# Kernel optimization log

Hardware: AMD Instinct MI355X
Metric: run time of the kernel (lower is better)

## Reference

```python
import jax, jax.numpy as jnp
import numpy as np

H = 100
EPS = 1e-5


def _ln(x, g, b):
    m = jnp.mean(x, axis=-1, keepdims=True)
    v = jnp.mean((x - m) ** 2, axis=-1, keepdims=True)
    return (x - m) / jnp.sqrt(v + EPS) * g + b


def _enc(x, W, b, g, be):
    # Linear -> Tanh -> LayerNorm
    return _ln(jnp.tanh(x @ W + b), g, be)


def setup_inputs() -> dict:
    key = jax.random.key(0)
    ks = jax.random.split(key, 16)
    B, N = 32768, 16
    obs_dim = 4 + 3 * N + 2 * (N - 1) + 2 * N  # 114
    d = {
        'inputs': jax.random.normal(ks[0], (B, obs_dim), dtype=jnp.float32),
        'agent_num': N,
        'sW': jax.random.normal(ks[1], (4, H), dtype=jnp.float32) * 0.5,
        'sb': jnp.zeros((H,), jnp.float32),
        'sg': jnp.ones((H,), jnp.float32),
        'sbe': jnp.zeros((H,), jnp.float32),
        'oW': jax.random.normal(ks[2], (2, H), dtype=jnp.float32) * 0.5,
        'ob': jnp.zeros((H,), jnp.float32),
        'og': jnp.ones((H,), jnp.float32),
        'obe': jnp.zeros((H,), jnp.float32),
        'lW': jax.random.normal(ks[3], (3, H), dtype=jnp.float32) * 0.5,
        'lb': jnp.zeros((H,), jnp.float32),
        'lg': jnp.ones((H,), jnp.float32),
        'lbe': jnp.zeros((H,), jnp.float32),
        'gW': jax.random.normal(ks[4], (2, H), dtype=jnp.float32) * 0.5,
        'gb': jnp.zeros((H,), jnp.float32),
        'gg': jnp.ones((H,), jnp.float32),
        'gbe': jnp.zeros((H,), jnp.float32),
        'Ac': jax.random.normal(ks[5], (H, H), dtype=jnp.float32) * 0.1,
        'Lc': jax.random.normal(ks[6], (H, H), dtype=jnp.float32) * 0.1,
        'fcW': jax.random.normal(ks[7], (H, H), dtype=jnp.float32) * 0.1,
        'fcb': jnp.zeros((H,), jnp.float32),
        'fcg': jnp.ones((H,), jnp.float32),
        'fcbe': jnp.zeros((H,), jnp.float32),
        'f1W': jax.random.normal(ks[8], (4 * H, H), dtype=jnp.float32) * 0.05,
        'f1b': jnp.zeros((H,), jnp.float32),
        'f1g': jnp.ones((H,), jnp.float32),
        'f1be': jnp.zeros((H,), jnp.float32),
        'f2W': jax.random.normal(ks[9], (H, H), dtype=jnp.float32) * 0.1,
        'f2b': jnp.zeros((H,), jnp.float32),
        'f2g': jnp.ones((H,), jnp.float32),
        'f2be': jnp.zeros((H,), jnp.float32),
    }
    return d


def reference(inputs, agent_num, sW, sb, sg, sbe, oW, ob, og, obe, lW, lb, lg, lbe, gW, gb, gg, gbe, Ac, Lc, fcW, fcb, fcg, fcbe, f1W, f1b, f1g, f1be, f2W, f2b, f2g, f2be):
    N = agent_num
    B = inputs.shape[0]
    self_emb = _enc(inputs[:, :4], sW, sb, sg, sbe)  # [B,H]
    lm = inputs[:, 4:4 + 3 * N].reshape(B, N, 3)
    off = 4 + 3 * N
    oth = inputs[:, off:off + 2 * (N - 1)].reshape(B, N - 1, 2)
    off2 = off + 2 * (N - 1)
    gl = inputs[:, off2:off2 + 2 * N].reshape(B, N, 2)
    oth_e = _enc(oth, oW, ob, og, obe)    # [B,N-1,H]
    lm_e = _enc(lm, lW, lb, lg, lbe)      # [B,N,H]
    gl_e = _enc(gl, gW, gb, gg, gbe)      # [B,N,H]
    qa = self_emb @ Ac                    # [B,H]
    ql = self_emb @ Lc                    # [B,H] (also used for goal: bug preserved from source)
    alpha_a = jax.nn.softmax(jnp.einsum('bh,bnh->bn', qa, oth_e), axis=1)
    va = jnp.einsum('bn,bnh->bh', alpha_a, oth_e)
    alpha_l = jax.nn.softmax(jnp.einsum('bh,bnh->bn', ql, lm_e), axis=1)
    vl = jnp.einsum('bn,bnh->bh', alpha_l, lm_e)
    alpha_g = jax.nn.softmax(jnp.einsum('bh,bnh->bn', ql, gl_e), axis=1)
    vg = jnp.einsum('bn,bnh->bh', alpha_g, gl_e)
    gi = _enc(self_emb, fcW, fcb, fcg, fcbe)
    x = jnp.concatenate([gi, va, vl, vg], axis=1)  # [B,4H]
    h = _enc(x, f1W, f1b, f1g, f1be)
    return _enc(h, f2W, f2b, f2g, f2be)
```

## Files before the change

kernel.cpp:

```cpp
#include <hip/hip_runtime.h>
#include <math.h>

#define OBS 114
#define ROWS_PER_BLOCK 16
#define BSTRIDE 104

__device__ __forceinline__ float fast_tanh(float x) {
    float e = __expf(2.0f * x);
    return 1.0f - 2.0f * __builtin_amdgcn_rcpf(e + 1.0f);
}

template<int CTRL>
__device__ __forceinline__ float dpp_add(float x) {
    int y = __builtin_amdgcn_update_dpp(0, __float_as_int(x), CTRL, 0xF, 0xF, true);
    return x + __int_as_float(y);
}
__device__ __forceinline__ float row16_sum(float x) {
    x = dpp_add<0xB1>(x);
    x = dpp_add<0x4E>(x);
    x = dpp_add<0x124>(x);
    x = dpp_add<0x128>(x);
    return x;
}
__device__ __forceinline__ float f4c(const float4& v, int j) {
    return j==0?v.x: j==1?v.y: j==2?v.z: v.w;
}

__global__ __launch_bounds__(256) void repack_kernel(
    const float* __restrict__ Ac, const float* __restrict__ Lc,
    const float* __restrict__ fcW, const float* __restrict__ f1W,
    const float* __restrict__ f2W, float* __restrict__ ws)
{
    int tid = blockIdx.x*256 + threadIdx.x;
    if (tid >= 800*128) return;
    int krow = tid >> 7;
    int idx  = tid & 127;
    int j = idx >> 3, i = idx & 7;
    int h = j + 16*i;
    const float* src; int k;
    if (krow < 100)      { src = Ac;  k = krow; }
    else if (krow < 200) { src = Lc;  k = krow-100; }
    else if (krow < 300) { src = fcW; k = krow-200; }
    else if (krow < 700) { src = f1W; k = krow-300; }
    else                 { src = f2W; k = krow-700; }
    float v = (i < 7 && h < 100) ? src[k*100 + h] : 0.f;
    ws[tid] = v;
}

template<int NK4>
__device__ __forceinline__ void mm16(const float* __restrict__ Wp,
    const float (*sbuf)[BSTRIDE], int R0, int R1, int j, float acc[7][2])
{
    const float* wp = Wp + j*8;
#pragma unroll 2
    for (int k4 = 0; k4 < NK4; ++k4) {
        float4 xa = *(const float4*)&sbuf[R0][k4*4];
        float4 xb = *(const float4*)&sbuf[R1][k4*4];
#pragma unroll
        for (int jj=0;jj<4;++jj) {
            const float* w8 = wp + (size_t)(k4*4+jj)*128;
            float4 wlo = *(const float4*)w8;
            float4 whi = *(const float4*)(w8+4);
            float w[7] = {wlo.x,wlo.y,wlo.z,wlo.w,whi.x,whi.y,whi.z};
            float xka = f4c(xa,jj), xkb = f4c(xb,jj);
#pragma unroll
            for (int i=0;i<7;++i) {
                acc[i][0] = fmaf(xka, w[i], acc[i][0]);
                acc[i][1] = fmaf(xkb, w[i], acc[i][1]);
            }
        }
    }
}

template<int K, int NA>
__device__ __forceinline__ void attn16(
    const float* __restrict__ W, const float* __restrict__ bb,
    const float* __restrict__ gp, const float* __restrict__ bep,
    const float* __restrict__ in, int xoff,
    float (*sbuf)[BSTRIDE],
    int rowAc, int rowBc, int RA, int RB,
    const float qacc[7][2],
    const int hc[7], const float msk[7])
{
    float w[K][7], bias[7], g[7], be[7];
#pragma unroll
    for (int i=0;i<7;++i) {
#pragma unroll
        for (int k=0;k<K;++k) w[k][i] = W[k*100 + hc[i]] * msk[i];
        bias[i] = bb[hc[i]] * msk[i];
        g[i]    = gp[hc[i]] * msk[i];
        be[i]   = bep[hc[i]];
    }
    float qg[2][7], C1[2];
#pragma unroll
    for (int b=0;b<2;++b) {
        float c = 0.f;
#pragma unroll
        for (int i=0;i<7;++i) { qg[b][i] = qacc[i][b]*g[i]; c += qg[b][i]; }
        C1[b] = row16_sum(c);
    }
    const float* xr0 = in + (size_t)rowAc*OBS + xoff;
    const float* xr1 = in + (size_t)rowBc*OBS + xoff;
    float s[2] = {0.f,0.f}, bacc[2] = {0.f,0.f};
    float A[2][7];
#pragma unroll
    for (int b=0;b<2;++b)
#pragma unroll
        for (int i=0;i<7;++i) A[b][i]=0.f;

#pragma unroll 1
    for (int n=0;n<NA;++n) {
        float x0[K], x1[K];
#pragma unroll
        for (int k=0;k<K;++k) { x0[k] = xr0[n*K+k]; x1[k] = xr1[n*K+k]; }
        float t[2][7], sa[2], sq[2], sd[2];
#pragma unroll
        for (int b=0;b<2;++b) { sa[b]=0.f; sq[b]=0.f; sd[b]=0.f; }
#pragma unroll
        for (int i=0;i<7;++i) {
#pragma unroll
            for (int b=0;b<2;++b) {
                float a = bias[i];
#pragma unroll
                for (int k=0;k<K;++k) a = fmaf(b ? x1[k] : x0[k], w[k][i], a);
                float tt = fast_tanh(a);
                t[b][i] = tt;
                sa[b] += tt;
                sq[b] = fmaf(tt,tt,sq[b]);
                sd[b] = fmaf(qg[b][i],tt,sd[b]);
            }
        }
#pragma unroll
        for (int b=0;b<2;++b) { sa[b]=row16_sum(sa[b]); sq[b]=row16_sum(sq[b]); sd[b]=row16_sum(sd[b]); }
#pragma unroll
        for (int b=0;b<2;++b) {
            float mean = sa[b]*0.01f;
            float var  = fmaf(sq[b],0.01f,-mean*mean);
            float rinv = __builtin_amdgcn_rsqf(var + 1e-5f);
            float logit = (sd[b]-mean*C1[b])*rinv;
            float wgt = __expf(fminf(logit,80.f));
            s[b] += wgt;
            float wr = wgt*rinv;
            bacc[b] = fmaf(wr,mean,bacc[b]);
#pragma unroll
            for (int i=0;i<7;++i) A[b][i] = fmaf(wr,t[b][i],A[b][i]);
        }
    }
#pragma unroll
    for (int b=0;b<2;++b) {
        int R = b ? RB : RA;
        float inv = __builtin_amdgcn_rcpf(s[b]);
#pragma unroll
        for (int i=0;i<7;++i)
            if (msk[i]>0.f) sbuf[R][hc[i]] = fmaf(g[i], (A[b][i]-bacc[b])*inv, be[i]);
    }
}

__device__ __forceinline__ void ln_pair(const float acc[7][2],
    const float* __restrict__ bp, const float* __restrict__ gp, const float* __restrict__ bep,
    const int hc[7], const float msk[7], float outv[2][7])
{
    float bias[7], g[7], be[7];
#pragma unroll
    for (int i=0;i<7;++i) { bias[i]=bp[hc[i]]*msk[i]; g[i]=gp[hc[i]]; be[i]=bep[hc[i]]; }
    float t[2][7], sa[2], sq[2];
#pragma unroll
    for (int b=0;b<2;++b) { sa[b]=0.f; sq[b]=0.f; }
#pragma unroll
    for (int i=0;i<7;++i) {
#pragma unroll
        for (int b=0;b<2;++b) {
            float tt = fast_tanh(acc[i][b] + bias[i]);
            t[b][i] = tt; sa[b] += tt*msk[i]; sq[b] = fmaf(tt*msk[i],tt,sq[b]);
        }
    }
#pragma unroll
    for (int b=0;b<2;++b) { sa[b]=row16_sum(sa[b]); sq[b]=row16_sum(sq[b]); }
#pragma unroll
    for (int b=0;b<2;++b) {
        float mean = sa[b]*0.01f;
        float var  = fmaf(sq[b],0.01f,-mean*mean);
        float rinv = __builtin_amdgcn_rsqf(var + 1e-5f);
#pragma unroll
        for (int i=0;i<7;++i) outv[b][i] = fmaf((t[b][i]-mean)*rinv, g[i], be[i]);
    }
}

__global__ __launch_bounds__(128, 4)
void obs_encoder_kernel(const float* __restrict__ in,
    const float* __restrict__ sW, const float* __restrict__ sb, const float* __restrict__ sg, const float* __restrict__ sbe,
    const float* __restrict__ oW, const float* __restrict__ ob, const float* __restrict__ og, const float* __restrict__ obe,
    const float* __restrict__ lW, const float* __restrict__ lb, const float* __restrict__ lg, const float* __restrict__ lbe,
    const float* __restrict__ gW, const float* __restrict__ gb, const float* __restrict__ gg_, const float* __restrict__ gbe,
    const float* __restrict__ fcb, const float* __restrict__ fcg, const float* __restrict__ fcbe,
    const float* __restrict__ f1b, const float* __restrict__ f1g, const float* __restrict__ f1be,
    const float* __restrict__ f2b, const float* __restrict__ f2g, const float* __restrict__ f2be,
    const float* __restrict__ wsf,
    float* __restrict__ out, int B)
{
    const int lane = threadIdx.x & 63;
    const int wv   = threadIdx.x >> 6;
    const int j    = lane & 15;
    const int rw   = lane >> 4;
    const int rowBase = blockIdx.x*ROWS_PER_BLOCK + wv*8;
    const int rowA = rowBase + rw;
    const int rowB = rowBase + 4 + rw;
    const int RA = wv*8 + rw, RB = RA + 4;
    const int rowAc = min(rowA, B-1), rowBc = min(rowB, B-1);

    int hc[7]; float msk[7];
#pragma unroll
    for (int i=0;i<7;++i) {
        int h = j + 16*i;
        bool v = h < 100;
        hc[i] = v ? h : 99;
        msk[i] = v ? 1.f : 0.f;
    }

    __shared__ __align__(16) float sbuf[ROWS_PER_BLOCK][BSTRIDE];

    const float* Acp = wsf;
    const float* Lcp = wsf + 12800;
    const float* fcp = wsf + 25600;
    const float* f1p = wsf + 38400;
    const float* f2p = wsf + 89600;

    {
        float w[4][7], bias[7], g[7], be[7];
#pragma unroll
        for (int i=0;i<7;++i) {
#pragma unroll
            for (int k=0;k<4;++k) w[k][i] = sW[k*100 + hc[i]] * msk[i];
            bias[i] = sb[hc[i]] * msk[i]; g[i] = sg[hc[i]]; be[i] = sbe[hc[i]];
        }
        const float* xr0 = in + (size_t)rowAc*OBS;
        const float* xr1 = in + (size_t)rowBc*OBS;
        float x[2][4];
#pragma unroll
        for (int k=0;k<4;++k) { x[0][k]=xr0[k]; x[1][k]=xr1[k]; }
        float t[2][7], sa[2], sq[2];
#pragma unroll
        for (int b=0;b<2;++b) { sa[b]=0.f; sq[b]=0.f; }
#pragma unroll
        for (int i=0;i<7;++i) {
#pragma unroll
            for (int b=0;b<2;++b) {
                float a = bias[i];
#pragma unroll
                for (int k=0;k<4;++k) a = fmaf(x[b][k], w[k][i], a);
                float tt = fast_tanh(a);
                t[b][i] = tt; sa[b] += tt*msk[i]; sq[b] = fmaf(tt*msk[i],tt,sq[b]);
            }
        }
#pragma unroll
        for (int b=0;b<2;++b) { sa[b]=row16_sum(sa[b]); sq[b]=row16_sum(sq[b]); }
#pragma unroll
        for (int b=0;b<2;++b) {
            int R = b ? RB : RA;
            float mean = sa[b]*0.01f;
            float var  = fmaf(sq[b],0.01f,-mean*mean);
            float rinv = __builtin_amdgcn_rsqf(var + 1e-5f);
#pragma unroll
            for (int i=0;i<7;++i)
                if (msk[i] > 0.f) sbuf[R][hc[i]] = fmaf((t[b][i]-mean)*rinv, g[i], be[i]);
        }
    }

    float accA[7][2], accL[7][2], accF[7][2];
#pragma unroll
    for (int i=0;i<7;++i) { accA[i][0]=accA[i][1]=accL[i][0]=accL[i][1]=accF[i][0]=accF[i][1]=0.f; }
    mm16<25>(Acp, sbuf, RA, RB, j, accA);
    mm16<25>(Lcp, sbuf, RA, RB, j, accL);
    mm16<25>(fcp, sbuf, RA, RB, j, accF);

    float f1a[7][2];
#pragma unroll
    for (int i=0;i<7;++i) { f1a[i][0]=0.f; f1a[i][1]=0.f; }

    {
        float outv[2][7];
        ln_pair(accF, fcb, fcg, fcbe, hc, msk, outv);
#pragma unroll
        for (int b=0;b<2;++b) {
            int R = b ? RB : RA;
#pragma unroll
            for (int i=0;i<7;++i)
                if (msk[i] > 0.f) sbuf[R][hc[i]] = outv[b][i];
        }
    }
    mm16<25>(f1p, sbuf, RA, RB, j, f1a);

    attn16<2,15>(oW, ob, og,  obe, in, 52, sbuf, rowAc, rowBc, RA, RB, accA, hc, msk);
    mm16<25>(f1p + 100*128, sbuf, RA, RB, j, f1a);
    attn16<3,16>(lW, lb, lg,  lbe, in, 4,  sbuf, rowAc, rowBc, RA, RB, accL, hc, msk);
    mm16<25>(f1p + 200*128, sbuf, RA, RB, j, f1a);
    attn16<2,16>(gW, gb, gg_, gbe, in, 82, sbuf, rowAc, rowBc, RA, RB, accL, hc, msk);
    mm16<25>(f1p + 300*128, sbuf, RA, RB, j, f1a);

    {
        float outv[2][7];
        ln_pair(f1a, f1b, f1g, f1be, hc, msk, outv);
#pragma unroll
        for (int b=0;b<2;++b) {
            int R = b ? RB : RA;
#pragma unroll
            for (int i=0;i<7;++i)
                if (msk[i] > 0.f) sbuf[R][hc[i]] = outv[b][i];
        }
    }

    {
        float acc[7][2];
#pragma unroll
        for (int i=0;i<7;++i) { acc[i][0]=0.f; acc[i][1]=0.f; }
        mm16<25>(f2p, sbuf, RA, RB, j, acc);
        float outv[2][7];
        ln_pair(acc, f2b, f2g, f2be, hc, msk, outv);
#pragma unroll
        for (int b=0;b<2;++b) {
            int row = b ? rowB : rowA;
            if (row < B) {
#pragma unroll
                for (int i=0;i<7;++i)
                    if (msk[i] > 0.f)
                        out[(size_t)row*100 + hc[i]] = outv[b][i];
            }
        }
    }
}

extern "C" void kernel_launch(void* const* d_in, const int* in_sizes, int n_in,
                              void* d_out, int out_size, void* d_ws, size_t ws_size,
                              hipStream_t stream) {
    const float* in  = (const float*)d_in[0];
    const float* sW  = (const float*)d_in[2];
    const float* sb  = (const float*)d_in[3];
    const float* sg  = (const float*)d_in[4];
    const float* sbe = (const float*)d_in[5];
    const float* oW  = (const float*)d_in[6];
    const float* ob  = (const float*)d_in[7];
    const float* og  = (const float*)d_in[8];
    const float* obe = (const float*)d_in[9];
    const float* lW  = (const float*)d_in[10];
    const float* lb  = (const float*)d_in[11];
    const float* lg  = (const float*)d_in[12];
    const float* lbe = (const float*)d_in[13];
    const float* gW  = (const float*)d_in[14];
    const float* gb  = (const float*)d_in[15];
    const float* gg  = (const float*)d_in[16];
    const float* gbe = (const float*)d_in[17];
    const float* Ac  = (const float*)d_in[18];
    const float* Lc  = (const float*)d_in[19];
    const float* fcW = (const float*)d_in[20];
    const float* fcb = (const float*)d_in[21];
    const float* fcg = (const float*)d_in[22];
    const float* fcbe= (const float*)d_in[23];
    const float* f1W = (const float*)d_in[24];
    const float* f1b = (const float*)d_in[25];
    const float* f1g = (const float*)d_in[26];
    const float* f1be= (const float*)d_in[27];
    const float* f2W = (const float*)d_in[28];
    const float* f2b = (const float*)d_in[29];
    const float* f2g = (const float*)d_in[30];
    const float* f2be= (const float*)d_in[31];
    float* out = (float*)d_out;
    float* wsf = (float*)d_ws;

    int B = in_sizes[0] / OBS;
    repack_kernel<<<(800*128 + 255)/256, 256, 0, stream>>>(Ac, Lc, fcW, f1W, f2W, wsf);
    int blocks = (B + ROWS_PER_BLOCK - 1) / ROWS_PER_BLOCK;
    obs_encoder_kernel<<<blocks, 128, 0, stream>>>(in,
        sW, sb, sg, sbe, oW, ob, og, obe, lW, lb, lg, lbe, gW, gb, gg, gbe,
        fcb, fcg, fcbe, f1b, f1g, f1be, f2b, f2g, f2be,
        wsf, out, B);
}
```

Baseline: 369.4 us.

## Use packed v2f FMAs, fuse three 100x100 matmuls, single-wave blocks

Converts the per-thread matmul, attention and layernorm inner loops to 2-wide float vectors so the compiler can emit packed FMA instructions (v_pk_fma_f32) and halve the FMA instruction count. The Ac, Lc and fcW matmuls are fused into one pass that reads each shared-memory input element once for all three weight matrices. Blocks shrink from two waves to one wave of 8 rows, which changes occupancy and the shared-memory footprint per block. The fused matmul needs more live accumulator registers, which may increase register pressure or cause spills.

```diff
diff --git a/kernel.cpp b/kernel.cpp
--- a/kernel.cpp
+++ b/kernel.cpp
@@ -2,8 +2,12 @@
 #include <math.h>
 
 #define OBS 114
-#define ROWS_PER_BLOCK 16
+#define ROWS_PER_BLOCK 8
 #define BSTRIDE 104
+
+typedef float v2f __attribute__((ext_vector_type(2)));
+__device__ __forceinline__ v2f v2fma(v2f a, v2f b, v2f c) { return __builtin_elementwise_fma(a, b, c); }
+__device__ __forceinline__ v2f vsplat(float x) { v2f r; r.x = x; r.y = x; return r; }
 
 __device__ __forceinline__ float fast_tanh(float x) {
     float e = __expf(2.0f * x);
@@ -48,8 +52,8 @@
 }
 
 template<int NK4>
-__device__ __forceinline__ void mm16(const float* __restrict__ Wp,
-    const float (*sbuf)[BSTRIDE], int R0, int R1, int j, float acc[7][2])
+__device__ __forceinline__ void mm16p(const float* __restrict__ Wp,
+    const float (*sbuf)[BSTRIDE], int R0, int R1, int j, v2f acc2[4][2])
 {
     const float* wp = Wp + j*8;
 #pragma unroll 2
@@ -61,12 +65,47 @@
             const float* w8 = wp + (size_t)(k4*4+jj)*128;
             float4 wlo = *(const float4*)w8;
             float4 whi = *(const float4*)(w8+4);
-            float w[7] = {wlo.x,wlo.y,wlo.z,wlo.w,whi.x,whi.y,whi.z};
-            float xka = f4c(xa,jj), xkb = f4c(xb,jj);
-#pragma unroll
-            for (int i=0;i<7;++i) {
-                acc[i][0] = fmaf(xka, w[i], acc[i][0]);
-                acc[i][1] = fmaf(xkb, w[i], acc[i][1]);
+            v2f w2[4] = {{wlo.x,wlo.y},{wlo.z,wlo.w},{whi.x,whi.y},{whi.z,whi.w}};
+            v2f xs0 = vsplat(f4c(xa,jj));
+            v2f xs1 = vsplat(f4c(xb,jj));
+#pragma unroll
+            for (int p=0;p<4;++p) {
+                acc2[p][0] = v2fma(xs0, w2[p], acc2[p][0]);
+                acc2[p][1] = v2fma(xs1, w2[p], acc2[p][1]);
+            }
+        }
+    }
+}
+
+template<int NK4>
+__device__ __forceinline__ void mm16x3(const float* __restrict__ W1,
+    const float* __restrict__ W2, const float* __restrict__ W3,
+    const float (*sbuf)[BSTRIDE], int R0, int R1, int j,
+    v2f a1[4][2], v2f a2[4][2], v2f a3[4][2])
+{
+    const float* p1 = W1 + j*8;
+    const float* p2 = W2 + j*8;
+    const float* p3 = W3 + j*8;
+#pragma unroll 2
+    for (int k4 = 0; k4 < NK4; ++k4) {
+        float4 xa = *(const float4*)&sbuf[R0][k4*4];
+        float4 xb = *(const float4*)&sbuf[R1][k4*4];
+#pragma unroll
+        for (int jj=0;jj<4;++jj) {
+            size_t off = (size_t)(k4*4+jj)*128;
+            float4 u1 = *(const float4*)(p1+off), v1 = *(const float4*)(p1+off+4);
+            float4 u2 = *(const float4*)(p2+off), v2 = *(const float4*)(p2+off+4);
+            float4 u3 = *(const float4*)(p3+off), v3 = *(const float4*)(p3+off+4);
+            v2f w1p[4] = {{u1.x,u1.y},{u1.z,u1.w},{v1.x,v1.y},{v1.z,v1.w}};
+            v2f w2p[4] = {{u2.x,u2.y},{u2.z,u2.w},{v2.x,v2.y},{v2.z,v2.w}};
+            v2f w3p[4] = {{u3.x,u3.y},{u3.z,u3.w},{v3.x,v3.y},{v3.z,v3.w}};
+            v2f xs0 = vsplat(f4c(xa,jj));
+            v2f xs1 = vsplat(f4c(xb,jj));
+#pragma unroll
+            for (int p=0;p<4;++p) {
+                a1[p][0]=v2fma(xs0,w1p[p],a1[p][0]); a1[p][1]=v2fma(xs1,w1p[p],a1[p][1]);
+                a2[p][0]=v2fma(xs0,w2p[p],a2[p][0]); a2[p][1]=v2fma(xs1,w2p[p],a2[p][1]);
+                a3[p][0]=v2fma(xs0,w3p[p],a3[p][0]); a3[p][1]=v2fma(xs1,w3p[p],a3[p][1]);
             }
         }
     }
@@ -79,56 +118,75 @@
     const float* __restrict__ in, int xoff,
     float (*sbuf)[BSTRIDE],
     int rowAc, int rowBc, int RA, int RB,
-    const float qacc[7][2],
+    const v2f qacc[4][2],
     const int hc[7], const float msk[7])
 {
-    float w[K][7], bias[7], g[7], be[7];
-#pragma unroll
-    for (int i=0;i<7;++i) {
-#pragma unroll
-        for (int k=0;k<K;++k) w[k][i] = W[k*100 + hc[i]] * msk[i];
-        bias[i] = bb[hc[i]] * msk[i];
-        g[i]    = gp[hc[i]] * msk[i];
-        be[i]   = bep[hc[i]];
-    }
-    float qg[2][7], C1[2];
+    float g[7], be[7];
+#pragma unroll
+    for (int i=0;i<7;++i) { g[i] = gp[hc[i]]*msk[i]; be[i] = bep[hc[i]]; }
+    v2f w2[K][4], bias2[4], g2[4];
+#pragma unroll
+    for (int p=0;p<4;++p) {
+        int i0 = 2*p, i1 = 2*p+1;
+        bias2[p].x = bb[hc[i0]]*msk[i0];
+        bias2[p].y = (i1<7) ? bb[hc[i1]]*msk[i1] : 0.f;
+        g2[p].x = g[i0];
+        g2[p].y = (i1<7) ? g[i1] : 0.f;
+#pragma unroll
+        for (int k=0;k<K;++k) {
+            w2[k][p].x = W[k*100+hc[i0]]*msk[i0];
+            w2[k][p].y = (i1<7) ? W[k*100+hc[i1]]*msk[i1] : 0.f;
+        }
+    }
+    v2f qg2[2][4]; float C1[2];
 #pragma unroll
     for (int b=0;b<2;++b) {
-        float c = 0.f;
-#pragma unroll
-        for (int i=0;i<7;++i) { qg[b][i] = qacc[i][b]*g[i]; c += qg[b][i]; }
-        C1[b] = row16_sum(c);
+        v2f c2 = {0.f,0.f};
+#pragma unroll
+        for (int p=0;p<4;++p) { qg2[b][p] = qacc[p][b]*g2[p]; c2 += qg2[b][p]; }
+        C1[b] = row16_sum(c2.x + c2.y);
     }
     const float* xr0 = in + (size_t)rowAc*OBS + xoff;
     const float* xr1 = in + (size_t)rowBc*OBS + xoff;
     float s[2] = {0.f,0.f}, bacc[2] = {0.f,0.f};
-    float A[2][7];
+    v2f A2[2][4];
 #pragma unroll
     for (int b=0;b<2;++b)
 #pragma unroll
-        for (int i=0;i<7;++i) A[b][i]=0.f;
+        for (int p=0;p<4;++p) A2[b][p] = (v2f){0.f,0.f};
 
 #pragma unroll 1
     for (int n=0;n<NA;++n) {
-        float x0[K], x1[K];
-#pragma unroll
-        for (int k=0;k<K;++k) { x0[k] = xr0[n*K+k]; x1[k] = xr1[n*K+k]; }
-        float t[2][7], sa[2], sq[2], sd[2];
-#pragma unroll
-        for (int b=0;b<2;++b) { sa[b]=0.f; sq[b]=0.f; sd[b]=0.f; }
-#pragma unroll
-        for (int i=0;i<7;++i) {
-#pragma unroll
-            for (int b=0;b<2;++b) {
-                float a = bias[i];
-#pragma unroll
-                for (int k=0;k<K;++k) a = fmaf(b ? x1[k] : x0[k], w[k][i], a);
-                float tt = fast_tanh(a);
-                t[b][i] = tt;
-                sa[b] += tt;
-                sq[b] = fmaf(tt,tt,sq[b]);
-                sd[b] = fmaf(qg[b][i],tt,sd[b]);
-            }
+        float x[2][K];
+#pragma unroll
+        for (int k=0;k<K;++k) { x[0][k] = xr0[n*K+k]; x[1][k] = xr1[n*K+k]; }
+        v2f t2[2][4];
+        float sa[2], sq[2], sd[2];
+#pragma unroll
+        for (int b=0;b<2;++b) {
+            v2f a2[4];
+#pragma unroll
+            for (int p=0;p<4;++p) a2[p] = bias2[p];
+#pragma unroll
+            for (int k=0;k<K;++k) {
+                v2f xs = vsplat(x[b][k]);
+#pragma unroll
+                for (int p=0;p<4;++p) a2[p] = v2fma(xs, w2[k][p], a2[p]);
+            }
+            t2[b][0].x = fast_tanh(a2[0].x); t2[b][0].y = fast_tanh(a2[0].y);
+            t2[b][1].x = fast_tanh(a2[1].x); t2[b][1].y = fast_tanh(a2[1].y);
+            t2[b][2].x = fast_tanh(a2[2].x); t2[b][2].y = fast_tanh(a2[2].y);
+            t2[b][3].x = fast_tanh(a2[3].x); t2[b][3].y = 0.f;
+            v2f sa2 = {0.f,0.f}, sq2 = {0.f,0.f}, sd2 = {0.f,0.f};
+#pragma unroll
+            for (int p=0;p<4;++p) {
+                sa2 += t2[b][p];
+                sq2 = v2fma(t2[b][p], t2[b][p], sq2);
+                sd2 = v2fma(qg2[b][p], t2[b][p], sd2);
+            }
+            sa[b] = sa2.x + sa2.y;
+            sq[b] = sq2.x + sq2.y;
+            sd[b] = sd2.x + sd2.y;
         }
 #pragma unroll
         for (int b=0;b<2;++b) { sa[b]=row16_sum(sa[b]); sq[b]=row16_sum(sq[b]); sd[b]=row16_sum(sd[b]); }
@@ -142,8 +200,9 @@
             s[b] += wgt;
             float wr = wgt*rinv;
             bacc[b] = fmaf(wr,mean,bacc[b]);
-#pragma unroll
-            for (int i=0;i<7;++i) A[b][i] = fmaf(wr,t[b][i],A[b][i]);
+            v2f wrs = vsplat(wr);
+#pragma unroll
+            for (int p=0;p<4;++p) A2[b][p] = v2fma(wrs, t2[b][p], A2[b][p]);
         }
     }
 #pragma unroll
@@ -151,12 +210,14 @@
         int R = b ? RB : RA;
         float inv = __builtin_amdgcn_rcpf(s[b]);
 #pragma unroll
-        for (int i=0;i<7;++i)
-            if (msk[i]>0.f) sbuf[R][hc[i]] = fmaf(g[i], (A[b][i]-bacc[b])*inv, be[i]);
-    }
-}
-
-__device__ __forceinline__ void ln_pair(const float acc[7][2],
+        for (int i=0;i<7;++i) {
+            float Ai = (i&1) ? A2[b][i>>1].y : A2[b][i>>1].x;
+            if (msk[i]>0.f) sbuf[R][hc[i]] = fmaf(g[i], (Ai-bacc[b])*inv, be[i]);
+        }
+    }
+}
+
+__device__ __forceinline__ void ln_pairp(const v2f acc2[4][2],
     const float* __restrict__ bp, const float* __restrict__ gp, const float* __restrict__ bep,
     const int hc[7], const float msk[7], float outv[2][7])
 {
@@ -170,7 +231,8 @@
     for (int i=0;i<7;++i) {
 #pragma unroll
         for (int b=0;b<2;++b) {
-            float tt = fast_tanh(acc[i][b] + bias[i]);
+            float a = (i&1) ? acc2[i>>1][b].y : acc2[i>>1][b].x;
+            float tt = fast_tanh(a + bias[i]);
             t[b][i] = tt; sa[b] += tt*msk[i]; sq[b] = fmaf(tt*msk[i],tt,sq[b]);
         }
     }
@@ -186,7 +248,7 @@
     }
 }
 
-__global__ __launch_bounds__(128, 4)
+__global__ __launch_bounds__(64, 4)
 void obs_encoder_kernel(const float* __restrict__ in,
     const float* __restrict__ sW, const float* __restrict__ sb, const float* __restrict__ sg, const float* __restrict__ sbe,
     const float* __restrict__ oW, const float* __restrict__ ob, const float* __restrict__ og, const float* __restrict__ obe,
@@ -198,14 +260,13 @@
     const float* __restrict__ wsf,
     float* __restrict__ out, int B)
 {
-    const int lane = threadIdx.x & 63;
-    const int wv   = threadIdx.x >> 6;
+    const int lane = threadIdx.x;
     const int j    = lane & 15;
     const int rw   = lane >> 4;
-    const int rowBase = blockIdx.x*ROWS_PER_BLOCK + wv*8;
+    const int rowBase = blockIdx.x*ROWS_PER_BLOCK;
     const int rowA = rowBase + rw;
     const int rowB = rowBase + 4 + rw;
-    const int RA = wv*8 + rw, RB = RA + 4;
+    const int RA = rw, RB = 4 + rw;
     const int rowAc = min(rowA, B-1), rowBc = min(rowB, B-1);
 
     int hc[7]; float msk[7];
@@ -266,20 +327,19 @@
         }
     }
 
-    float accA[7][2], accL[7][2], accF[7][2];
-#pragma unroll
-    for (int i=0;i<7;++i) { accA[i][0]=accA[i][1]=accL[i][0]=accL[i][1]=accF[i][0]=accF[i][1]=0.f; }
-    mm16<25>(Acp, sbuf, RA, RB, j, accA);
-    mm16<25>(Lcp, sbuf, RA, RB, j, accL);
-    mm16<25>(fcp, sbuf, RA, RB, j, accF);
-
-    float f1a[7][2];
-#pragma unroll
-    for (int i=0;i<7;++i) { f1a[i][0]=0.f; f1a[i][1]=0.f; }
+    v2f accA[4][2], accL[4][2], accF[4][2], f1a[4][2];
+#pragma unroll
+    for (int p=0;p<4;++p)
+#pragma unroll
+        for (int b=0;b<2;++b) {
+            accA[p][b] = (v2f){0.f,0.f}; accL[p][b] = (v2f){0.f,0.f};
+            accF[p][b] = (v2f){0.f,0.f}; f1a[p][b]  = (v2f){0.f,0.f};
+        }
+    mm16x3<25>(Acp, Lcp, fcp, sbuf, RA, RB, j, accA, accL, accF);
 
     {
         float outv[2][7];
-        ln_pair(accF, fcb, fcg, fcbe, hc, msk, outv);
+        ln_pairp(accF, fcb, fcg, fcbe, hc, msk, outv);
 #pragma unroll
         for (int b=0;b<2;++b) {
             int R = b ? RB : RA;
@@ -288,18 +348,18 @@
                 if (msk[i] > 0.f) sbuf[R][hc[i]] = outv[b][i];
         }
     }
-    mm16<25>(f1p, sbuf, RA, RB, j, f1a);
+    mm16p<25>(f1p, sbuf, RA, RB, j, f1a);
 
     attn16<2,15>(oW, ob, og,  obe, in, 52, sbuf, rowAc, rowBc, RA, RB, accA, hc, msk);
-    mm16<25>(f1p + 100*128, sbuf, RA, RB, j, f1a);
+    mm16p<25>(f1p + 100*128, sbuf, RA, RB, j, f1a);
     attn16<3,16>(lW, lb, lg,  lbe, in, 4,  sbuf, rowAc, rowBc, RA, RB, accL, hc, msk);
-    mm16<25>(f1p + 200*128, sbuf, RA, RB, j, f1a);
+    mm16p<25>(f1p + 200*128, sbuf, RA, RB, j, f1a);
     attn16<2,16>(gW, gb, gg_, gbe, in, 82, sbuf, rowAc, rowBc, RA, RB, accL, hc, msk);
-    mm16<25>(f1p + 300*128, sbuf, RA, RB, j, f1a);
+    mm16p<25>(f1p + 300*128, sbuf, RA, RB, j, f1a);
 
     {
         float outv[2][7];
-        ln_pair(f1a, f1b, f1g, f1be, hc, msk, outv);
+        ln_pairp(f1a, f1b, f1g, f1be, hc, msk, outv);
 #pragma unroll
         for (int b=0;b<2;++b) {
             int R = b ? RB : RA;
@@ -310,12 +370,12 @@
     }
 
     {
-        float acc[7][2];
-#pragma unroll
-        for (int i=0;i<7;++i) { acc[i][0]=0.f; acc[i][1]=0.f; }
-        mm16<25>(f2p, sbuf, RA, RB, j, acc);
+        v2f accO[4][2];
+#pragma unroll
+        for (int p=0;p<4;++p) { accO[p][0]=(v2f){0.f,0.f}; accO[p][1]=(v2f){0.f,0.f}; }
+        mm16p<25>(f2p, sbuf, RA, RB, j, accO);
         float outv[2][7];
-        ln_pair(acc, f2b, f2g, f2be, hc, msk, outv);
+        ln_pairp(accO, f2b, f2g, f2be, hc, msk, outv);
 #pragma unroll
         for (int b=0;b<2;++b) {
             int row = b ? rowB : rowA;
@@ -369,7 +429,7 @@
     int B = in_sizes[0] / OBS;
     repack_kernel<<<(800*128 + 255)/256, 256, 0, stream>>>(Ac, Lc, fcW, f1W, f2W, wsf);
     int blocks = (B + ROWS_PER_BLOCK - 1) / ROWS_PER_BLOCK;
-    obs_encoder_kernel<<<blocks, 128, 0, stream>>>(in,
+    obs_encoder_kernel<<<blocks, 64, 0, stream>>>(in,
         sW, sb, sg, sbe, oW, ob, og, obe, lW, lb, lg, lbe, gW, gb, gg, gbe,
         fcb, fcg, fcbe, f1b, f1g, f1be, f2b, f2g, f2be,
         wsf, out, B);
```

Result: slower. 432.7 us (+17.1%).
